# Kernel optimization log

Measured on AMD Instinct MI355X. Metric: run time of the kernel, lower is better.

The kernel has to match this reference:

```python
import jax, jax.numpy as jnp
import numpy as np


def setup_inputs() -> dict:
    key = jax.random.key(0)
    ks = jax.random.split(key, 6)
    B, Tq, Tk = 4, 512, 512
    Q, K, C = 1024, 1024, 256
    query = jax.random.normal(ks[0], (B, Tq, Q), dtype=jnp.float32)
    kmat = jax.random.normal(ks[1], (B, Tk, K), dtype=jnp.float32)
    # Linear weights (torch nn.Linear stores [out, in]; we keep [in, out] for einsum)
    Wq = jax.random.normal(ks[2], (Q, C), dtype=jnp.float32) / np.sqrt(Q)
    Wk = jax.random.normal(ks[3], (K, C), dtype=jnp.float32) / np.sqrt(K)
    w_attn = jax.random.normal(ks[4], (C,), dtype=jnp.float32) / np.sqrt(C)
    b_attn = jax.random.normal(ks[5], (), dtype=jnp.float32) * 0.01
    return {"query": query, "key": kmat, "Wq": Wq, "Wk": Wk,
            "w_attn": w_attn, "b_attn": b_attn}


def reference(query, key, Wq, Wk, w_attn, b_attn):
    # Additive (Bahdanau) attention scores.
    # q2ctx: (B, Tq, C); k2ctx: (B, Tk, C)
    q2ctx = jnp.einsum('bqi,ic->bqc', query, Wq)
    k2ctx = jnp.einsum('bki,ic->bkc', key, Wk)
    # broadcast add -> (B, Tq, Tk, C), tanh, project to scalar and squeeze
    ctx = jnp.tanh(q2ctx[:, :, None, :] + k2ctx[:, None, :, :])
    scores = jnp.einsum('bqkc,c->bqk', ctx, w_attn) + b_attn
    return scores  # (B, Tq, Tk)
```

## Files before the change

### kernel.cpp

```cpp
#include <hip/hip_runtime.h>
#include <hip/hip_bf16.h>

#define M_ROWS 2048
#define KDIM   1024
#define CDIM   256
#define TQ     512
#define TK     512

#define GBM 64
#define GBN 32
#define GBK 32

#define SCALE2LOG2E 2.8853900817779268f

typedef __attribute__((ext_vector_type(8))) short short8;
typedef __attribute__((ext_vector_type(8))) unsigned short ushort8;
typedef __attribute__((ext_vector_type(4))) float floatx4;
typedef __attribute__((ext_vector_type(2))) float f32x2;

__device__ __forceinline__ short2 cvt2(float x, float y) {
    __hip_bfloat162 h = __float22bfloat162_rn(make_float2(x, y));
    short2 r;
    __builtin_memcpy(&r, &h, sizeof(r));
    return r;
}
__device__ __forceinline__ unsigned short f2bf1(float x) {
    return (unsigned short)cvt2(x, x).x;
}
__device__ __forceinline__ float bf2f(unsigned short u) {
    return __builtin_bit_cast(float, (unsigned)u << 16);
}
__device__ __forceinline__ f32x2 splat2(float x) { return (f32x2){x, x}; }

__global__ __launch_bounds__(256) void gemm_mfma_kernel(
    const float* __restrict__ Aq, const float* __restrict__ Ak,
    const float* __restrict__ Wq, const float* __restrict__ Wk,
    const float* __restrict__ w_attn,
    unsigned short* __restrict__ Eq, unsigned short* __restrict__ Ek)
{
    __shared__ short Ws[GBN][GBK + 8];

    const int z = blockIdx.z;
    const float* A = z ? Ak : Aq;
    const float* W = z ? Wk : Wq;
    unsigned short* E = z ? Ek : Eq;

    const int t    = threadIdx.x;
    const int lane = t & 63;
    const int wave = t >> 6;
    const int m0   = blockIdx.x * GBM;
    const int n0   = blockIdx.y * GBN;

    const int wr = t >> 3;
    const int wc = (t & 7) * 4;
    const int li = lane & 15;
    const int qd = lane >> 4;

    const int row = m0 + wave * 16 + li;
    const float* Arow = A + (size_t)row * KDIM + qd * 8;

    floatx4 acc0 = {0.f, 0.f, 0.f, 0.f};
    floatx4 acc1 = {0.f, 0.f, 0.f, 0.f};

    float4 pa0[2], pa1[2], pw[2];
    pa0[0] = *(const float4*)&Arow[0];
    pa1[0] = *(const float4*)&Arow[4];
    pw[0]  = *(const float4*)&W[(size_t)wr * CDIM + n0 + wc];
    pa0[1] = *(const float4*)&Arow[GBK];
    pa1[1] = *(const float4*)&Arow[GBK + 4];
    pw[1]  = *(const float4*)&W[(size_t)(GBK + wr) * CDIM + n0 + wc];

    for (int it = 0; it < KDIM / GBK; ++it) {
        const int s = it & 1;
        __syncthreads();
        short2 u0 = cvt2(pw[s].x, pw[s].y), u1 = cvt2(pw[s].z, pw[s].w);
        Ws[wc + 0][wr] = u0.x;
        Ws[wc + 1][wr] = u0.y;
        Ws[wc + 2][wr] = u1.x;
        Ws[wc + 3][wr] = u1.y;
        short2 p0 = cvt2(pa0[s].x, pa0[s].y), p1 = cvt2(pa0[s].z, pa0[s].w);
        short2 p2 = cvt2(pa1[s].x, pa1[s].y), p3 = cvt2(pa1[s].z, pa1[s].w);
        short8 bv = { p0.x, p0.y, p1.x, p1.y, p2.x, p2.y, p3.x, p3.y };
        __syncthreads();
        if (it + 2 < KDIM / GBK) {
            const int k0 = (it + 2) * GBK;
            pa0[s] = *(const float4*)&Arow[k0];
            pa1[s] = *(const float4*)&Arow[k0 + 4];
            pw[s]  = *(const float4*)&W[(size_t)(k0 + wr) * CDIM + n0 + wc];
        }
        short8 af0 = *(const short8*)&Ws[li][qd * 8];
        short8 af1 = *(const short8*)&Ws[16 + li][qd * 8];
        acc0 = __builtin_amdgcn_mfma_f32_16x16x32_bf16(af0, bv, acc0, 0, 0, 0);
        acc1 = __builtin_amdgcn_mfma_f32_16x16x32_bf16(af1, bv, acc1, 0, 0, 0);
    }

    #pragma unroll
    for (int r = 0; r < 4; ++r) {
        const int c0 = n0 + qd * 4 + r;
        const int c1 = c0 + 16;
        float s0 = z ? 1.0f : (-0.5f / w_attn[c0]);
        float s1 = z ? 1.0f : (-0.5f / w_attn[c1]);
        float v0 = __builtin_amdgcn_exp2f(acc0[r] * SCALE2LOG2E) * s0;
        float v1 = __builtin_amdgcn_exp2f(acc1[r] * SCALE2LOG2E) * s1;
        E[(size_t)c0 * M_ROWS + row] = f2bf1(v0);
        E[(size_t)c1 * M_ROWS + row] = f2bf1(v1);
    }
}

__global__ __launch_bounds__(256) void bahdanau_kernel(
    const unsigned short* __restrict__ Eqs, const unsigned short* __restrict__ Ek,
    const float* __restrict__ w_attn, const float* __restrict__ b_attn,
    float* __restrict__ out)
{
    __shared__ float qs[64][36];
    __shared__ float ks[64][36];
    __shared__ __align__(16) float sl[CDIM];
    __shared__ float partial[4];

    const int t  = threadIdx.x;
    const int b  = blockIdx.z;
    const int q0 = blockIdx.x * 32;
    const int k0 = blockIdx.y * 32;
    const int gq = b * TQ + q0;
    const int gk = b * TK + k0;
    const int tq = (t >> 4) * 2;
    const int tk = (t & 15) * 2;

    const int lr = t >> 2;
    const int lc = (t & 3) * 8;

    {
        float wv = w_attn[t];
        sl[t] = -0.5f / wv;
        float sum = wv;
        #pragma unroll
        for (int o = 32; o >= 1; o >>= 1) sum += __shfl_down(sum, o);
        if ((t & 63) == 0) partial[t >> 6] = sum;
    }

    ushort8 qu = *(const ushort8*)&Eqs[(size_t)lr * M_ROWS + gq + lc];
    ushort8 ku = *(const ushort8*)&Ek [(size_t)lr * M_ROWS + gk + lc];

    f32x2 accA = {0.f, 0.f};
    f32x2 accB = {0.f, 0.f};

    for (int ch = 0; ch < 4; ++ch) {
        __syncthreads();
        *(float4*)&qs[lr][lc]     = make_float4(bf2f(qu[0]), bf2f(qu[1]), bf2f(qu[2]), bf2f(qu[3]));
        *(float4*)&qs[lr][lc + 4] = make_float4(bf2f(qu[4]), bf2f(qu[5]), bf2f(qu[6]), bf2f(qu[7]));
        *(float4*)&ks[lr][lc]     = make_float4(bf2f(ku[0]), bf2f(ku[1]), bf2f(ku[2]), bf2f(ku[3]));
        *(float4*)&ks[lr][lc + 4] = make_float4(bf2f(ku[4]), bf2f(ku[5]), bf2f(ku[6]), bf2f(ku[7]));
        __syncthreads();
        if (ch < 3) {
            const int c1 = (ch + 1) * 64;
            qu = *(const ushort8*)&Eqs[(size_t)(c1 + lr) * M_ROWS + gq + lc];
            ku = *(const ushort8*)&Ek [(size_t)(c1 + lr) * M_ROWS + gk + lc];
        }
        const int cb = ch * 64;
        #pragma unroll
        for (int cc = 0; cc < 64; cc += 4) {
            float4 s4 = *(const float4*)&sl[cb + cc];
            f32x2 q1 = *(const f32x2*)&qs[cc + 0][tq];
            f32x2 q2 = *(const f32x2*)&qs[cc + 1][tq];
            f32x2 q3 = *(const f32x2*)&qs[cc + 2][tq];
            f32x2 q4 = *(const f32x2*)&qs[cc + 3][tq];
            f32x2 k1 = *(const f32x2*)&ks[cc + 0][tk];
            f32x2 k2 = *(const f32x2*)&ks[cc + 1][tk];
            f32x2 k3 = *(const f32x2*)&ks[cc + 2][tk];
            f32x2 k4 = *(const f32x2*)&ks[cc + 3][tk];
            {
                f32x2 f1 = __builtin_elementwise_fma(splat2(q1.x), k1, splat2(s4.x));
                f32x2 f2 = __builtin_elementwise_fma(splat2(q2.x), k2, splat2(s4.y));
                f32x2 f3 = __builtin_elementwise_fma(splat2(q3.x), k3, splat2(s4.z));
                f32x2 f4 = __builtin_elementwise_fma(splat2(q4.x), k4, splat2(s4.w));
                f32x2 p12 = f1 * f2, p34 = f3 * f4;
                f32x2 s12 = f1 + f2, s34 = f3 + f4;
                f32x2 num = __builtin_elementwise_fma(s12, p34, s34 * p12);
                f32x2 den = p12 * p34;
                f32x2 r = {__builtin_amdgcn_rcpf(den.x), __builtin_amdgcn_rcpf(den.y)};
                accA = __builtin_elementwise_fma(num, r, accA);
            }
            {
                f32x2 f1 = __builtin_elementwise_fma(splat2(q1.y), k1, splat2(s4.x));
                f32x2 f2 = __builtin_elementwise_fma(splat2(q2.y), k2, splat2(s4.y));
                f32x2 f3 = __builtin_elementwise_fma(splat2(q3.y), k3, splat2(s4.z));
                f32x2 f4 = __builtin_elementwise_fma(splat2(q4.y), k4, splat2(s4.w));
                f32x2 p12 = f1 * f2, p34 = f3 * f4;
                f32x2 s12 = f1 + f2, s34 = f3 + f4;
                f32x2 num = __builtin_elementwise_fma(s12, p34, s34 * p12);
                f32x2 den = p12 * p34;
                f32x2 r = {__builtin_amdgcn_rcpf(den.x), __builtin_amdgcn_rcpf(den.y)};
                accB = __builtin_elementwise_fma(num, r, accB);
            }
        }
    }

    const float bias2 = *b_attn + partial[0] + partial[1] + partial[2] + partial[3];
    float* o = out + ((size_t)b * TQ + q0 + tq) * TK + k0 + tk;
    *(float2*)&o[0]  = make_float2(accA.x + bias2, accA.y + bias2);
    *(float2*)&o[TK] = make_float2(accB.x + bias2, accB.y + bias2);
}

extern "C" void kernel_launch(void* const* d_in, const int* in_sizes, int n_in,
                              void* d_out, int out_size, void* d_ws, size_t ws_size,
                              hipStream_t stream) {
    const float* query  = (const float*)d_in[0];
    const float* key    = (const float*)d_in[1];
    const float* Wq     = (const float*)d_in[2];
    const float* Wk     = (const float*)d_in[3];
    const float* w_attn = (const float*)d_in[4];
    const float* b_attn = (const float*)d_in[5];
    float* out = (float*)d_out;

    unsigned short* Eqs = (unsigned short*)d_ws;
    unsigned short* Ek  = Eqs + (size_t)CDIM * M_ROWS;

    dim3 gemm_grid(M_ROWS / GBM, CDIM / GBN, 2);
    gemm_mfma_kernel<<<gemm_grid, 256, 0, stream>>>(query, key, Wq, Wk, w_attn, Eqs, Ek);

    dim3 main_grid(TQ / 32, TK / 32, 4);
    bahdanau_kernel<<<main_grid, 256, 0, stream>>>(Eqs, Ek, w_attn, b_attn, out);
}
```

Measured before the change: 110.8 us.

## Pre-transpose weights to bf16 and drop LDS staging in projection GEMM

Adds a small kernel that transposes Wq and Wk into bf16 [C][K] layout in the workspace. The projection GEMM then loads MFMA weight fragments straight from global memory, with no shared-memory staging and no barriers, in a simple unrolled loop. This removes per-iteration syncs and the scattered LDS transposed writes. In exchange it adds one kernel launch and drops the explicit double-buffered prefetch, so the loop relies on the unroll and the compiler to hide load latency.

New measurement: 126.3 us. 14.0% more time.

```diff
diff --git a/kernel.cpp b/kernel.cpp
--- a/kernel.cpp
+++ b/kernel.cpp
@@ -32,17 +32,39 @@
 }
 __device__ __forceinline__ f32x2 splat2(float x) { return (f32x2){x, x}; }
 
+__global__ __launch_bounds__(256) void wt_kernel(
+    const float* __restrict__ Wq, const float* __restrict__ Wk,
+    unsigned short* __restrict__ WTq, unsigned short* __restrict__ WTk)
+{
+    __shared__ float tile[32][36];
+    const float* W = blockIdx.z ? Wk : Wq;
+    unsigned short* WT = blockIdx.z ? WTk : WTq;
+    const int k0 = blockIdx.x * 32;
+    const int c0 = blockIdx.y * 32;
+    const int t  = threadIdx.x;
+    const int row = t >> 3;
+    const int col = (t & 7) * 4;
+
+    float4 v = *(const float4*)&W[(size_t)(k0 + row) * CDIM + c0 + col];
+    *(float4*)&tile[row][col] = v;
+    __syncthreads();
+    const int cr = t >> 3;
+    const int kc = (t & 7) * 4;
+    short2 a = cvt2(tile[kc + 0][cr], tile[kc + 1][cr]);
+    short2 b = cvt2(tile[kc + 2][cr], tile[kc + 3][cr]);
+    short4 o = make_short4(a.x, a.y, b.x, b.y);
+    *(short4*)&WT[(size_t)(c0 + cr) * KDIM + k0 + kc] = o;
+}
+
 __global__ __launch_bounds__(256) void gemm_mfma_kernel(
     const float* __restrict__ Aq, const float* __restrict__ Ak,
-    const float* __restrict__ Wq, const float* __restrict__ Wk,
+    const unsigned short* __restrict__ WTq, const unsigned short* __restrict__ WTk,
     const float* __restrict__ w_attn,
     unsigned short* __restrict__ Eq, unsigned short* __restrict__ Ek)
 {
-    __shared__ short Ws[GBN][GBK + 8];
-
     const int z = blockIdx.z;
     const float* A = z ? Ak : Aq;
-    const float* W = z ? Wk : Wq;
+    const unsigned short* WT = z ? WTk : WTq;
     unsigned short* E = z ? Ek : Eq;
 
     const int t    = threadIdx.x;
@@ -50,46 +72,26 @@
     const int wave = t >> 6;
     const int m0   = blockIdx.x * GBM;
     const int n0   = blockIdx.y * GBN;
-
-    const int wr = t >> 3;
-    const int wc = (t & 7) * 4;
-    const int li = lane & 15;
-    const int qd = lane >> 4;
+    const int li   = lane & 15;
+    const int qd   = lane >> 4;
 
     const int row = m0 + wave * 16 + li;
-    const float* Arow = A + (size_t)row * KDIM + qd * 8;
+    const float* Arow          = A  + (size_t)row * KDIM + qd * 8;
+    const unsigned short* Wrow0 = WT + (size_t)(n0 + li) * KDIM + qd * 8;
+    const unsigned short* Wrow1 = WT + (size_t)(n0 + 16 + li) * KDIM + qd * 8;
 
     floatx4 acc0 = {0.f, 0.f, 0.f, 0.f};
     floatx4 acc1 = {0.f, 0.f, 0.f, 0.f};
 
-    float4 pa0[2], pa1[2], pw[2];
-    pa0[0] = *(const float4*)&Arow[0];
-    pa1[0] = *(const float4*)&Arow[4];
-    pw[0]  = *(const float4*)&W[(size_t)wr * CDIM + n0 + wc];
-    pa0[1] = *(const float4*)&Arow[GBK];
-    pa1[1] = *(const float4*)&Arow[GBK + 4];
-    pw[1]  = *(const float4*)&W[(size_t)(GBK + wr) * CDIM + n0 + wc];
-
-    for (int it = 0; it < KDIM / GBK; ++it) {
-        const int s = it & 1;
-        __syncthreads();
-        short2 u0 = cvt2(pw[s].x, pw[s].y), u1 = cvt2(pw[s].z, pw[s].w);
-        Ws[wc + 0][wr] = u0.x;
-        Ws[wc + 1][wr] = u0.y;
-        Ws[wc + 2][wr] = u1.x;
-        Ws[wc + 3][wr] = u1.y;
-        short2 p0 = cvt2(pa0[s].x, pa0[s].y), p1 = cvt2(pa0[s].z, pa0[s].w);
-        short2 p2 = cvt2(pa1[s].x, pa1[s].y), p3 = cvt2(pa1[s].z, pa1[s].w);
+    #pragma unroll 4
+    for (int k0 = 0; k0 < KDIM; k0 += GBK) {
+        float4 a0 = *(const float4*)&Arow[k0];
+        float4 a1 = *(const float4*)&Arow[k0 + 4];
+        short8 af0 = *(const short8*)&Wrow0[k0];
+        short8 af1 = *(const short8*)&Wrow1[k0];
+        short2 p0 = cvt2(a0.x, a0.y), p1 = cvt2(a0.z, a0.w);
+        short2 p2 = cvt2(a1.x, a1.y), p3 = cvt2(a1.z, a1.w);
         short8 bv = { p0.x, p0.y, p1.x, p1.y, p2.x, p2.y, p3.x, p3.y };
-        __syncthreads();
-        if (it + 2 < KDIM / GBK) {
-            const int k0 = (it + 2) * GBK;
-            pa0[s] = *(const float4*)&Arow[k0];
-            pa1[s] = *(const float4*)&Arow[k0 + 4];
-            pw[s]  = *(const float4*)&W[(size_t)(k0 + wr) * CDIM + n0 + wc];
-        }
-        short8 af0 = *(const short8*)&Ws[li][qd * 8];
-        short8 af1 = *(const short8*)&Ws[16 + li][qd * 8];
         acc0 = __builtin_amdgcn_mfma_f32_16x16x32_bf16(af0, bv, acc0, 0, 0, 0);
         acc1 = __builtin_amdgcn_mfma_f32_16x16x32_bf16(af1, bv, acc1, 0, 0, 0);
     }
@@ -214,9 +216,14 @@
 
     unsigned short* Eqs = (unsigned short*)d_ws;
     unsigned short* Ek  = Eqs + (size_t)CDIM * M_ROWS;
+    unsigned short* WTq = Ek  + (size_t)CDIM * M_ROWS;
+    unsigned short* WTk = WTq + (size_t)CDIM * KDIM;
+
+    dim3 wt_grid(KDIM / 32, CDIM / 32, 2);
+    wt_kernel<<<wt_grid, 256, 0, stream>>>(Wq, Wk, WTq, WTk);
 
     dim3 gemm_grid(M_ROWS / GBM, CDIM / GBN, 2);
-    gemm_mfma_kernel<<<gemm_grid, 256, 0, stream>>>(query, key, Wq, Wk, w_attn, Eqs, Ek);
+    gemm_mfma_kernel<<<gemm_grid, 256, 0, stream>>>(query, key, WTq, WTk, w_attn, Eqs, Ek);
 
     dim3 main_grid(TQ / 32, TK / 32, 4);
     bahdanau_kernel<<<main_grid, 256, 0, stream>>>(Eqs, Ek, w_attn, b_attn, out);
```

## Stage 128-wide K chunks of W in LDS to cut GEMM barriers

Applied to the files above, without the earlier changes.

The projection GEMM now stages W in 128-wide K chunks instead of 32, so each thread converts four float4s per chunk. This cuts the number of __syncthreads pairs from 32 to 8. Activation loads now go straight to registers inside an unrolled 4-step MFMA loop, with no register double-buffering of A. That loses the explicit prefetch of A and relies on the compiler to hoist the loads, and it enlarges the LDS tile.

Result: no change. 112.4 us (+1.4%).

```diff
diff --git a/kernel.cpp b/kernel.cpp
--- a/kernel.cpp
+++ b/kernel.cpp
@@ -9,7 +9,7 @@
 
 #define GBM 64
 #define GBN 32
-#define GBK 32
+#define CK  128
 
 #define SCALE2LOG2E 2.8853900817779268f
 
@@ -38,7 +38,7 @@
     const float* __restrict__ w_attn,
     unsigned short* __restrict__ Eq, unsigned short* __restrict__ Ek)
 {
-    __shared__ short Ws[GBN][GBK + 8];
+    __shared__ short Ws[GBN][CK + 8];
 
     const int z = blockIdx.z;
     const float* A = z ? Ak : Aq;
@@ -50,48 +50,54 @@
     const int wave = t >> 6;
     const int m0   = blockIdx.x * GBM;
     const int n0   = blockIdx.y * GBN;
-
-    const int wr = t >> 3;
-    const int wc = (t & 7) * 4;
-    const int li = lane & 15;
-    const int qd = lane >> 4;
+    const int li   = lane & 15;
+    const int qd   = lane >> 4;
 
     const int row = m0 + wave * 16 + li;
     const float* Arow = A + (size_t)row * KDIM + qd * 8;
 
+    const int kr = t >> 1;
+    const int h  = t & 1;
+    const float* Wst = W + (size_t)kr * CDIM + n0 + h * 16;
+
     floatx4 acc0 = {0.f, 0.f, 0.f, 0.f};
     floatx4 acc1 = {0.f, 0.f, 0.f, 0.f};
 
-    float4 pa0[2], pa1[2], pw[2];
-    pa0[0] = *(const float4*)&Arow[0];
-    pa1[0] = *(const float4*)&Arow[4];
-    pw[0]  = *(const float4*)&W[(size_t)wr * CDIM + n0 + wc];
-    pa0[1] = *(const float4*)&Arow[GBK];
-    pa1[1] = *(const float4*)&Arow[GBK + 4];
-    pw[1]  = *(const float4*)&W[(size_t)(GBK + wr) * CDIM + n0 + wc];
-
-    for (int it = 0; it < KDIM / GBK; ++it) {
-        const int s = it & 1;
-        __syncthreads();
-        short2 u0 = cvt2(pw[s].x, pw[s].y), u1 = cvt2(pw[s].z, pw[s].w);
-        Ws[wc + 0][wr] = u0.x;
-        Ws[wc + 1][wr] = u0.y;
-        Ws[wc + 2][wr] = u1.x;
-        Ws[wc + 3][wr] = u1.y;
-        short2 p0 = cvt2(pa0[s].x, pa0[s].y), p1 = cvt2(pa0[s].z, pa0[s].w);
-        short2 p2 = cvt2(pa1[s].x, pa1[s].y), p3 = cvt2(pa1[s].z, pa1[s].w);
-        short8 bv = { p0.x, p0.y, p1.x, p1.y, p2.x, p2.y, p3.x, p3.y };
-        __syncthreads();
-        if (it + 2 < KDIM / GBK) {
-            const int k0 = (it + 2) * GBK;
-            pa0[s] = *(const float4*)&Arow[k0];
-            pa1[s] = *(const float4*)&Arow[k0 + 4];
-            pw[s]  = *(const float4*)&W[(size_t)(k0 + wr) * CDIM + n0 + wc];
-        }
-        short8 af0 = *(const short8*)&Ws[li][qd * 8];
-        short8 af1 = *(const short8*)&Ws[16 + li][qd * 8];
-        acc0 = __builtin_amdgcn_mfma_f32_16x16x32_bf16(af0, bv, acc0, 0, 0, 0);
-        acc1 = __builtin_amdgcn_mfma_f32_16x16x32_bf16(af1, bv, acc1, 0, 0, 0);
+    float4 wreg[4];
+    #pragma unroll
+    for (int u = 0; u < 4; ++u) wreg[u] = *(const float4*)&Wst[4 * u];
+
+    for (int ck = 0; ck < KDIM / CK; ++ck) {
+        __syncthreads();
+        #pragma unroll
+        for (int u = 0; u < 4; ++u) {
+            short2 e0 = cvt2(wreg[u].x, wreg[u].y);
+            short2 e1 = cvt2(wreg[u].z, wreg[u].w);
+            const int c = h * 16 + 4 * u;
+            Ws[c + 0][kr] = e0.x;
+            Ws[c + 1][kr] = e0.y;
+            Ws[c + 2][kr] = e1.x;
+            Ws[c + 3][kr] = e1.y;
+        }
+        __syncthreads();
+        if (ck + 1 < KDIM / CK) {
+            const float* Wn = Wst + (size_t)(ck + 1) * CK * CDIM;
+            #pragma unroll
+            for (int u = 0; u < 4; ++u) wreg[u] = *(const float4*)&Wn[4 * u];
+        }
+        #pragma unroll
+        for (int s = 0; s < 4; ++s) {
+            const int kk = ck * CK + s * 32;
+            float4 a0 = *(const float4*)&Arow[kk];
+            float4 a1 = *(const float4*)&Arow[kk + 4];
+            short8 af0 = *(const short8*)&Ws[li][s * 32 + qd * 8];
+            short8 af1 = *(const short8*)&Ws[16 + li][s * 32 + qd * 8];
+            short2 p0 = cvt2(a0.x, a0.y), p1 = cvt2(a0.z, a0.w);
+            short2 p2 = cvt2(a1.x, a1.y), p3 = cvt2(a1.z, a1.w);
+            short8 bv = { p0.x, p0.y, p1.x, p1.y, p2.x, p2.y, p3.x, p3.y };
+            acc0 = __builtin_amdgcn_mfma_f32_16x16x32_bf16(af0, bv, acc0, 0, 0, 0);
+            acc1 = __builtin_amdgcn_mfma_f32_16x16x32_bf16(af1, bv, acc1, 0, 0, 0);
+        }
     }
 
     #pragma unroll
```
